# Optimization experiments

Measured on AMD Instinct MI355X. Metric: run time of the kernel, lower is better.

## Reference

```python
import jax, jax.numpy as jnp
import numpy as np
import math

B, S, D = 2, 2048, 2048
H, KVH, WIN = 16, 4, 256
HD = D // H            # 128
QPER = H // KVH        # 4


def setup_inputs() -> dict:
    key = jax.random.key(0)
    ks = jax.random.split(key, 9)
    s = lambda k, shp: jax.random.normal(k, shp, dtype=jnp.float32) * 0.02
    return {
        "x": jax.random.normal(ks[0], (B, S, D), dtype=jnp.float32),
        "Wq": s(ks[1], (D, D)),            "bq": jnp.zeros((D,), jnp.float32),
        "Wk": s(ks[2], (D, KVH * HD)),      "bk": jnp.zeros((KVH * HD,), jnp.float32),
        "Wv": s(ks[3], (D, KVH * HD)),      "bv": jnp.zeros((KVH * HD,), jnp.float32),
        "Wo": s(ks[4], (D, D)),            "bo": jnp.zeros((D,), jnp.float32),
    }


def reference(x, Wq, bq, Wk, bk, Wv, bv, Wo, bo):
    b, s, _ = x.shape
    # projections
    Q = (x @ Wq + bq).reshape(b, s, H, HD).transpose(0, 2, 1, 3)     # [b,H,s,hd]
    K = (x @ Wk + bk).reshape(b, s, KVH, HD).transpose(0, 2, 1, 3)   # [b,kvh,s,hd]
    V = (x @ Wv + bv).reshape(b, s, KVH, HD).transpose(0, 2, 1, 3)   # [b,kvh,s,hd]
    # GQA grouping: head h = g*QPER + q
    Qg = Q.reshape(b, KVH, QPER, s, HD)                               # [b,g,q,s,hd]
    scores = jnp.einsum('bgqsd,bgtd->bgqst', Qg, K)                   # [b,g,q,s,s]
    i = jnp.arange(s)[:, None]
    j = jnp.arange(s)[None, :]
    keep = (j <= i) & (j >= i - WIN + 1)                              # [s,s]
    scores = jnp.where(keep, scores, -jnp.inf)
    A = jax.nn.softmax(scores / math.sqrt(HD), axis=-1)
    O = jnp.einsum('bgqst,bgtd->bgqsd', A, V)                         # [b,g,q,s,hd]
    O = O.reshape(b, H, s, HD).transpose(0, 2, 1, 3).reshape(b, s, D)
    return O @ Wo + bo
```

## Files before the change

### kernel.cpp

```cpp
#include <hip/hip_runtime.h>
#include <hip/hip_bf16.h>
#include <math.h>

typedef __bf16 bf16_t;
typedef bf16_t bf16x8 __attribute__((ext_vector_type(8)));
typedef bf16_t bf16x4 __attribute__((ext_vector_type(4)));
typedef float  f32x4  __attribute__((ext_vector_type(4)));

#define NB    2
#define SEQ   2048
#define DIM   2048
#define NHEAD 16
#define NKVH  4
#define HDIM  128
#define WINSZ 256
#define KVD   512
#define QKVN  3072
#define MROWS 4096

__device__ __forceinline__ void async_copy16(const void* g, void* lds) {
    __builtin_amdgcn_global_load_lds(
        (const __attribute__((address_space(1))) void*)g,
        (__attribute__((address_space(3))) void*)lds,
        16, 0, 0);
}

__global__ __launch_bounds__(256) void preprocess(
    const float* __restrict__ x,  const float* __restrict__ Wq,
    const float* __restrict__ bq, const float* __restrict__ Wk,
    const float* __restrict__ bk, const float* __restrict__ Wv,
    const float* __restrict__ bv, const float* __restrict__ Wo,
    bf16_t* __restrict__ xb, bf16_t* __restrict__ WqkvT,
    bf16_t* __restrict__ WoT, float* __restrict__ bqkv) {
    __shared__ float tile[32][33];
    const int tid = threadIdx.x;
    int bid = blockIdx.x;
    if (bid < 8192) {
        int i = (bid * 256 + tid) * 4;
        float4 v = *(const float4*)(x + i);
        bf16x4 o;
        o[0] = (bf16_t)v.x; o[1] = (bf16_t)v.y; o[2] = (bf16_t)v.z; o[3] = (bf16_t)v.w;
        *(bf16x4*)(xb + i) = o;
        return;
    }
    bid -= 8192;
    const float* src; bf16_t* dst; int N;
    if (bid < 4096)       { src = Wq; dst = WqkvT;                          N = DIM; }
    else if (bid < 5120)  { src = Wk; dst = WqkvT + (size_t)DIM * DIM;      N = KVD; bid -= 4096; }
    else if (bid < 6144)  { src = Wv; dst = WqkvT + (size_t)(DIM+KVD)*DIM;  N = KVD; bid -= 5120; }
    else if (bid < 10240) { src = Wo; dst = WoT;                            N = DIM; bid -= 6144; }
    else {
        int i = (bid - 10240) * 256 + tid;
        if (i < QKVN) {
            float v = (i < DIM) ? bq[i] : ((i < DIM + KVD) ? bk[i - DIM] : bv[i - DIM - KVD]);
            bqkv[i] = v;
        }
        return;
    }
    const int K = DIM;
    int ntile = N / 32;
    int n0 = (bid % ntile) * 32, k0 = (bid / ntile) * 32;
    int tx = tid & 31, ty = tid >> 5;
    for (int r = ty; r < 32; r += 8)
        tile[r][tx] = src[(size_t)(k0 + r) * N + n0 + tx];
    __syncthreads();
    for (int r = ty; r < 32; r += 8)
        dst[(size_t)(n0 + r) * K + k0 + tx] = (bf16_t)tile[tx][r];
}

__global__ __launch_bounds__(256) void transpose_v(const bf16_t* __restrict__ QKV,
                                                   bf16_t* __restrict__ Vtb) {
    __shared__ bf16_t t[32][33];
    int tx = threadIdx.x & 31, ty = threadIdx.x >> 5;
    int jb = blockIdx.x, c0 = blockIdx.y * 32, b = blockIdx.z;
    int j0 = jb * 32;
    for (int r = ty; r < 32; r += 8)
        t[r][tx] = QKV[((size_t)(b * SEQ) + j0 + r) * QKVN + (DIM + KVD) + c0 + tx];
    __syncthreads();
    int g = c0 >> 7, dl = c0 & 127;
    bf16_t* outb = Vtb + (((size_t)(b * NKVH) + g) * 64 + jb) * 4096;
    for (int r = ty; r < 32; r += 8)
        outb[(dl + r) * 32 + tx] = t[tx][r];
}

template <int BM, int BN, typename OutT>
__global__ __launch_bounds__(512, 1) void gemm8p(const bf16_t* __restrict__ A,
                                                 const bf16_t* __restrict__ Bt,
                                                 const float* __restrict__ bias,
                                                 OutT* __restrict__ C,
                                                 int M, int N, int K, float qs, int qcols) {
    constexpr int ASLOTS = BM / 16;
    constexpr int BSLOTS = BN / 16;
    constexpr int MF   = BM / 32;
    constexpr int NF   = BN / 64;
    constexpr int AHALF = BM * 32;
    constexpr int BHALF = BN * 32;
    constexpr int BUFSZ = 2 * (AHALF + BHALF);
    __shared__ bf16_t lds[2 * BUFSZ];

    const int tid  = threadIdx.x;
    const int wave = tid >> 6;
    const int lane = tid & 63;
    const int lg = lane >> 4, lc = lane & 15;
    const int wr = wave >> 2, wc = wave & 3;

    const int nbn  = N / BN;
    const int nblk = (M / BM) * nbn;
    const int qq   = nblk >> 3;
    const int swz  = (blockIdx.x & 7) * qq + (blockIdx.x >> 3);
    const long brow = (long)(swz / nbn) * BM;
    const long bcol = (long)(swz % nbn) * BN;

    const int aiss = (ASLOTS - wave + 7) >> 3;
    const int biss = (BSLOTS - wave + 7) >> 3;
    const int miss = aiss + biss;

    f32x4 acc[MF][NF] = {};

    auto stage = [&](int buf, int p, int kt) {
        const int kcol = kt * 64 + p * 32;
        const int srow = lane >> 2;
        const int sch  = lane & 3;
        {
            bf16_t* d = lds + buf * BUFSZ + p * AHALF;
#pragma unroll
            for (int s = wave; s < ASLOTS; s += 8) {
                int row = s * 16 + srow;
                int ch  = sch ^ ((row >> 1) & 3);
                async_copy16(A + (brow + row) * (long)K + kcol + ch * 8, d + s * 512);
            }
        }
        {
            bf16_t* d = lds + buf * BUFSZ + 2 * AHALF + p * BHALF;
#pragma unroll
            for (int s = wave; s < BSLOTS; s += 8) {
                int row = s * 16 + srow;
                int ch  = sch ^ ((row >> 1) & 3);
                async_copy16(Bt + (bcol + row) * (long)K + kcol + ch * 8, d + s * 512);
            }
        }
    };

    stage(0, 0, 0);
    stage(0, 1, 0);

    const int NT = K >> 6;
    const int cswz = (lg ^ ((lc >> 1) & 3)) * 8;
    for (int t = 0; t < NT; ++t) {
#pragma unroll
        for (int p = 0; p < 2; ++p) {
            if (t == NT - 1 && p == 1) {
                asm volatile("s_waitcnt vmcnt(0)" ::: "memory");
            } else if (miss == 4) {
                asm volatile("s_waitcnt vmcnt(4)" ::: "memory");
            } else if (miss == 3) {
                asm volatile("s_waitcnt vmcnt(3)" ::: "memory");
            } else {
                asm volatile("s_waitcnt vmcnt(2)" ::: "memory");
            }
            __builtin_amdgcn_s_barrier();
            asm volatile("" ::: "memory");
            const bf16_t* Ab = lds + (t & 1) * BUFSZ + p * AHALF;
            const bf16_t* Bb = lds + (t & 1) * BUFSZ + 2 * AHALF + p * BHALF;
            bf16x8 af[MF], bv[NF];
#pragma unroll
            for (int m = 0; m < MF; ++m)
                af[m] = *(const bf16x8*)(Ab + (wr * (BM / 2) + m * 16 + lc) * 32 + cswz);
#pragma unroll
            for (int n = 0; n < NF; ++n)
                bv[n] = *(const bf16x8*)(Bb + (wc * (BN / 4) + n * 16 + lc) * 32 + cswz);
            if (t + 1 < NT) stage((t + 1) & 1, p, t + 1);
            __builtin_amdgcn_s_setprio(1);
#pragma unroll
            for (int m = 0; m < MF; ++m)
#pragma unroll
                for (int n = 0; n < NF; ++n)
                    acc[m][n] = __builtin_amdgcn_mfma_f32_16x16x32_bf16(af[m], bv[n], acc[m][n], 0, 0, 0);
            __builtin_amdgcn_s_setprio(0);
        }
    }

#pragma unroll
    for (int n = 0; n < NF; ++n) {
        int gc = (int)bcol + wc * (BN / 4) + n * 16 + lc;
        float bvs = bias[gc];
        bool ds = gc < qcols;
#pragma unroll
        for (int m = 0; m < MF; ++m) {
            long gr = brow + wr * (BM / 2) + m * 16 + 4 * lg;
#pragma unroll
            for (int r = 0; r < 4; ++r) {
                float v = acc[m][n][r] + bvs;
                if (ds) v *= qs;
                C[(gr + r) * (long)N + gc] = (OutT)v;
            }
        }
    }
}

__global__ __launch_bounds__(256) void attn_kernel(const bf16_t* __restrict__ QKV,
                                                   const bf16_t* __restrict__ Vtb,
                                                   bf16_t* __restrict__ Ob) {
    __shared__ bf16_t Kls[2][32 * 128];
    __shared__ bf16_t Vls[2][128 * 32];
    __shared__ bf16_t Pls[4][32 * 40];

    const int wv   = threadIdx.x >> 6;
    const int lane = threadIdx.x & 63;
    const int lg = lane >> 4, lc = lane & 15;

    const int swb = (blockIdx.x & 7) * 64 + (blockIdx.x >> 3);
    const int ti = swb & 63;
    const int g  = (swb >> 6) & 3;
    const int b  = swb >> 8;
    const int h  = g * 4 + wv;
    const int i0 = ti * 32;
    bf16_t* P = &Pls[wv][0];

    bf16x8 qf[2][4];
#pragma unroll
    for (int sq = 0; sq < 2; ++sq) {
        const bf16_t* qp = QKV + ((size_t)(b * SEQ) + i0 + sq * 16 + lc) * QKVN + h * HDIM + lg * 8;
#pragma unroll
        for (int kk = 0; kk < 4; ++kk) qf[sq][kk] = *(const bf16x8*)(qp + kk * 32);
    }

    auto stage = [&](int buf, int jb) {
        const int j0s = jb * 32;
        const bf16_t* kgb = QKV + ((size_t)(b * SEQ) + j0s) * QKVN + DIM + g * HDIM;
#pragma unroll
        for (int ii = 0; ii < 2; ++ii) {
            int i = wv * 2 + ii;
            int row = i * 4 + (lane >> 4);
            int ch  = (lane & 15) ^ (row & 7);
            async_copy16(kgb + (size_t)row * QKVN + ch * 8, &Kls[buf][i * 512]);
        }
        const bf16_t* vgb = Vtb + (((size_t)(b * NKVH) + g) * 64 + jb) * 4096;
#pragma unroll
        for (int ii = 0; ii < 2; ++ii) {
            int i = wv * 2 + ii;
            int row = i * 16 + (lane >> 2);
            int ch  = (lane & 3) ^ ((row ^ (row >> 2)) & 3);
            async_copy16(vgb + row * 32 + ch * 8, &Vls[buf][i * 512]);
        }
    };

    float m_run[2] = {-1e30f, -1e30f}, l_run[2] = {0.f, 0.f};
    f32x4 oacc[2][8] = {};

    int jlo = i0 - (WINSZ - 1); if (jlo < 0) jlo = 0;
    const int jb0 = jlo >> 5;
    const int jb1 = (i0 + 31) >> 5;

    stage(0, jb0);

    for (int jb = jb0; jb <= jb1; ++jb) {
        const int j0 = jb * 32;
        const int cur = (jb - jb0) & 1;
        asm volatile("s_waitcnt vmcnt(0)" ::: "memory");
        __builtin_amdgcn_s_barrier();
        asm volatile("" ::: "memory");

        bf16x8 kf[2][4];
#pragma unroll
        for (int t = 0; t < 2; ++t)
#pragma unroll
            for (int kk = 0; kk < 4; ++kk) {
                int row = t * 16 + lc;
                int ch  = (kk * 4 + lg) ^ (row & 7);
                kf[t][kk] = *(const bf16x8*)(&Kls[cur][row * 128 + ch * 8]);
            }
        if (jb < jb1) stage(cur ^ 1, jb + 1);
        asm volatile("s_waitcnt lgkmcnt(0)" ::: "memory");
        __builtin_amdgcn_sched_barrier(0);

        f32x4 s[2][2];
        __builtin_amdgcn_s_setprio(1);
#pragma unroll
        for (int t = 0; t < 2; ++t)
#pragma unroll
            for (int sq = 0; sq < 2; ++sq) {
                f32x4 sv = {};
#pragma unroll
                for (int kk = 0; kk < 4; ++kk)
                    sv = __builtin_amdgcn_mfma_f32_16x16x32_bf16(kf[t][kk], qf[sq][kk], sv, 0, 0, 0);
                s[t][sq] = sv;
            }
        __builtin_amdgcn_s_setprio(0);

        const bool edge = (j0 < i0 - (WINSZ - 32)) || (j0 > i0 - 31);
        if (edge) {
#pragma unroll
            for (int t = 0; t < 2; ++t)
#pragma unroll
                for (int sq = 0; sq < 2; ++sq) {
                    int irow = i0 + sq * 16 + lc;
#pragma unroll
                    for (int r = 0; r < 4; ++r) {
                        int j = j0 + t * 16 + 4 * lg + r;
                        if (j > irow || j < irow - (WINSZ - 1)) s[t][sq][r] = -1e30f;
                    }
                }
        }
        float tmax[2];
#pragma unroll
        for (int sq = 0; sq < 2; ++sq) {
            float tm = fmaxf(fmaxf(fmaxf(s[0][sq][0], s[0][sq][1]), fmaxf(s[0][sq][2], s[0][sq][3])),
                             fmaxf(fmaxf(s[1][sq][0], s[1][sq][1]), fmaxf(s[1][sq][2], s[1][sq][3])));
            tm = fmaxf(tm, __shfl_xor(tm, 16, 64));
            tm = fmaxf(tm, __shfl_xor(tm, 32, 64));
            tmax[sq] = tm;
        }
        if (!__all(tmax[0] - m_run[0] <= 8.0f && tmax[1] - m_run[1] <= 8.0f)) {
#pragma unroll
            for (int sq = 0; sq < 2; ++sq) {
                float m_new = fmaxf(m_run[sq], tmax[sq]);
                float resc = __builtin_amdgcn_exp2f(m_run[sq] - m_new);
                l_run[sq] *= resc;
#pragma unroll
                for (int c = 0; c < 8; ++c) {
                    oacc[sq][c][0] *= resc; oacc[sq][c][1] *= resc;
                    oacc[sq][c][2] *= resc; oacc[sq][c][3] *= resc;
                }
                m_run[sq] = m_new;
            }
        }
        float psum[2] = {0.f, 0.f};
#pragma unroll
        for (int t = 0; t < 2; ++t)
#pragma unroll
            for (int sq = 0; sq < 2; ++sq) {
                bf16x4 pk;
#pragma unroll
                for (int r = 0; r < 4; ++r) {
                    float sv = s[t][sq][r];
                    float p = (edge && sv < -5e29f) ? 0.f : __builtin_amdgcn_exp2f(sv - m_run[sq]);
                    psum[sq] += p;
                    pk[r] = (bf16_t)p;
                }
                *(bf16x4*)(P + (sq * 16 + lc) * 40 + t * 16 + lg * 4) = pk;
            }
#pragma unroll
        for (int sq = 0; sq < 2; ++sq) {
            float ps = psum[sq];
            ps += __shfl_xor(ps, 16, 64);
            ps += __shfl_xor(ps, 32, 64);
            l_run[sq] += ps;
        }
        asm volatile("" ::: "memory");

        bf16x8 vf[8];
#pragma unroll
        for (int c = 0; c < 8; ++c) {
            int row = c * 16 + lc;
            int ch  = lg ^ ((row ^ (row >> 2)) & 3);
            vf[c] = *(const bf16x8*)(&Vls[cur][row * 32 + ch * 8]);
        }
        bf16x8 pf[2];
#pragma unroll
        for (int sq = 0; sq < 2; ++sq)
            pf[sq] = *(const bf16x8*)(P + (sq * 16 + lc) * 40 + lg * 8);

        __builtin_amdgcn_s_setprio(1);
#pragma unroll
        for (int c = 0; c < 8; ++c)
#pragma unroll
            for (int sq = 0; sq < 2; ++sq)
                oacc[sq][c] = __builtin_amdgcn_mfma_f32_16x16x32_bf16(vf[c], pf[sq], oacc[sq][c], 0, 0, 0);
        __builtin_amdgcn_s_setprio(0);
    }

#pragma unroll
    for (int sq = 0; sq < 2; ++sq) {
        const float inv = 1.f / l_run[sq];
#pragma unroll
        for (int c = 0; c < 8; ++c) {
            bf16x4 ov;
#pragma unroll
            for (int r = 0; r < 4; ++r) ov[r] = (bf16_t)(oacc[sq][c][r] * inv);
            *(bf16x4*)(Ob + ((size_t)(b * SEQ) + i0 + sq * 16 + lc) * DIM + h * HDIM + c * 16 + lg * 4) = ov;
        }
    }
}

extern "C" void kernel_launch(void* const* d_in, const int* in_sizes, int n_in,
                              void* d_out, int out_size, void* d_ws, size_t ws_size,
                              hipStream_t stream) {
    const float* x  = (const float*)d_in[0];
    const float* Wq = (const float*)d_in[1];
    const float* bq = (const float*)d_in[2];
    const float* Wk = (const float*)d_in[3];
    const float* bk = (const float*)d_in[4];
    const float* Wv = (const float*)d_in[5];
    const float* bv = (const float*)d_in[6];
    const float* Wo = (const float*)d_in[7];
    const float* bo = (const float*)d_in[8];
    float* out = (float*)d_out;

    char* ws = (char*)d_ws;
    bf16_t* xb    = (bf16_t*)(ws);
    bf16_t* WqkvT = (bf16_t*)(ws + (16u << 20));
    bf16_t* WoT   = (bf16_t*)(ws + (28u << 20));
    bf16_t* QKVb  = (bf16_t*)(ws + (36u << 20));
    float*  bqkv  = (float*) (ws + (60u << 20));
    bf16_t* Vtb   = WqkvT;
    bf16_t* Ob    = xb;

    const float qs = 0.12751707498038074f;

    preprocess<<<18444, 256, 0, stream>>>(x, Wq, bq, Wk, bk, Wv, bv, Wo,
                                          xb, WqkvT, WoT, bqkv);

    gemm8p<256, 192, bf16_t><<<dim3((MROWS / 256) * (QKVN / 192)), 512, 0, stream>>>(
        xb, WqkvT, bqkv, QKVb, MROWS, QKVN, DIM, qs, DIM);

    transpose_v<<<dim3(SEQ / 32, KVD / 32, NB), 256, 0, stream>>>(QKVb, Vtb);

    attn_kernel<<<dim3(NB * NKVH * (SEQ / 32)), 256, 0, stream>>>(QKVb, Vtb, Ob);

    gemm8p<128, 256, float><<<dim3((MROWS / 128) * (DIM / 256)), 512, 0, stream>>>(
        Ob, WoT, bo, out, MROWS, DIM, DIM, 1.0f, 0);
}
```

Baseline: 147.6 us.

## Replace large-tile GEMM with 128x128 triple-buffered multi-block GEMM

Both projection GEMMs move from one 512-thread block per CU with 256x192 or 128x256 tiles and double buffering to 256-thread blocks with 128x128 tiles, K-step 32, a three-stage LDS ring, and three blocks per CU. The goal is more blocks in flight and deeper prefetch to hide load latency, and better wave balance across CUs. The cost is lower per-block data reuse, so more global and L2 traffic per FLOP and more barriers per unit of work.

```diff
diff --git a/kernel.cpp b/kernel.cpp
--- a/kernel.cpp
+++ b/kernel.cpp
@@ -83,111 +83,79 @@
         outb[(dl + r) * 32 + tx] = t[tx][r];
 }
 
-template <int BM, int BN, typename OutT>
-__global__ __launch_bounds__(512, 1) void gemm8p(const bf16_t* __restrict__ A,
+template <typename OutT>
+__global__ __launch_bounds__(256, 3) void gemm3b(const bf16_t* __restrict__ A,
                                                  const bf16_t* __restrict__ Bt,
                                                  const float* __restrict__ bias,
                                                  OutT* __restrict__ C,
                                                  int M, int N, int K, float qs, int qcols) {
-    constexpr int ASLOTS = BM / 16;
-    constexpr int BSLOTS = BN / 16;
-    constexpr int MF   = BM / 32;
-    constexpr int NF   = BN / 64;
-    constexpr int AHALF = BM * 32;
-    constexpr int BHALF = BN * 32;
-    constexpr int BUFSZ = 2 * (AHALF + BHALF);
-    __shared__ bf16_t lds[2 * BUFSZ];
-
-    const int tid  = threadIdx.x;
-    const int wave = tid >> 6;
-    const int lane = tid & 63;
+    __shared__ bf16_t lds[3][8192];
+    const int tid = threadIdx.x, wave = tid >> 6, lane = tid & 63;
     const int lg = lane >> 4, lc = lane & 15;
-    const int wr = wave >> 2, wc = wave & 3;
-
-    const int nbn  = N / BN;
-    const int nblk = (M / BM) * nbn;
-    const int qq   = nblk >> 3;
-    const int swz  = (blockIdx.x & 7) * qq + (blockIdx.x >> 3);
-    const long brow = (long)(swz / nbn) * BM;
-    const long bcol = (long)(swz % nbn) * BN;
-
-    const int aiss = (ASLOTS - wave + 7) >> 3;
-    const int biss = (BSLOTS - wave + 7) >> 3;
-    const int miss = aiss + biss;
-
-    f32x4 acc[MF][NF] = {};
-
-    auto stage = [&](int buf, int p, int kt) {
-        const int kcol = kt * 64 + p * 32;
-        const int srow = lane >> 2;
-        const int sch  = lane & 3;
-        {
-            bf16_t* d = lds + buf * BUFSZ + p * AHALF;
-#pragma unroll
-            for (int s = wave; s < ASLOTS; s += 8) {
-                int row = s * 16 + srow;
-                int ch  = sch ^ ((row >> 1) & 3);
-                async_copy16(A + (brow + row) * (long)K + kcol + ch * 8, d + s * 512);
-            }
-        }
-        {
-            bf16_t* d = lds + buf * BUFSZ + 2 * AHALF + p * BHALF;
-#pragma unroll
-            for (int s = wave; s < BSLOTS; s += 8) {
-                int row = s * 16 + srow;
-                int ch  = sch ^ ((row >> 1) & 3);
-                async_copy16(Bt + (bcol + row) * (long)K + kcol + ch * 8, d + s * 512);
-            }
+    const int wr = wave >> 1, wc = wave & 1;
+    const int nbn = N >> 7, nblk = (M >> 7) * nbn, qq = nblk >> 3;
+    const int swz = (blockIdx.x & 7) * qq + (blockIdx.x >> 3);
+    const long brow = (long)(swz / nbn) << 7;
+    const long bcol = (long)(swz % nbn) << 7;
+    const int srow = tid >> 2;
+    const int sch  = tid & 3;
+    const int cswz = (lg ^ ((lc >> 1) & 3)) * 8;
+
+    f32x4 acc[4][4] = {};
+
+    auto stage = [&](int buf, int kt) {
+        const long kc = (long)kt * 32;
+#pragma unroll
+        for (int h = 0; h < 2; ++h) {
+            int row = h * 64 + srow;
+            int ch  = sch ^ ((row >> 1) & 3);
+            async_copy16(A + (brow + row) * (long)K + kc + ch * 8,
+                         &lds[buf][h * 2048 + tid * 8]);
+        }
+#pragma unroll
+        for (int h = 0; h < 2; ++h) {
+            int row = h * 64 + srow;
+            int ch  = sch ^ ((row >> 1) & 3);
+            async_copy16(Bt + (bcol + row) * (long)K + kc + ch * 8,
+                         &lds[buf][4096 + h * 2048 + tid * 8]);
         }
     };
 
-    stage(0, 0, 0);
-    stage(0, 1, 0);
-
-    const int NT = K >> 6;
-    const int cswz = (lg ^ ((lc >> 1) & 3)) * 8;
+    const int NT = K >> 5;
+    stage(0, 0);
+    stage(1, 1);
+
     for (int t = 0; t < NT; ++t) {
-#pragma unroll
-        for (int p = 0; p < 2; ++p) {
-            if (t == NT - 1 && p == 1) {
-                asm volatile("s_waitcnt vmcnt(0)" ::: "memory");
-            } else if (miss == 4) {
-                asm volatile("s_waitcnt vmcnt(4)" ::: "memory");
-            } else if (miss == 3) {
-                asm volatile("s_waitcnt vmcnt(3)" ::: "memory");
-            } else {
-                asm volatile("s_waitcnt vmcnt(2)" ::: "memory");
-            }
-            __builtin_amdgcn_s_barrier();
-            asm volatile("" ::: "memory");
-            const bf16_t* Ab = lds + (t & 1) * BUFSZ + p * AHALF;
-            const bf16_t* Bb = lds + (t & 1) * BUFSZ + 2 * AHALF + p * BHALF;
-            bf16x8 af[MF], bv[NF];
-#pragma unroll
-            for (int m = 0; m < MF; ++m)
-                af[m] = *(const bf16x8*)(Ab + (wr * (BM / 2) + m * 16 + lc) * 32 + cswz);
-#pragma unroll
-            for (int n = 0; n < NF; ++n)
-                bv[n] = *(const bf16x8*)(Bb + (wc * (BN / 4) + n * 16 + lc) * 32 + cswz);
-            if (t + 1 < NT) stage((t + 1) & 1, p, t + 1);
-            __builtin_amdgcn_s_setprio(1);
-#pragma unroll
-            for (int m = 0; m < MF; ++m)
-#pragma unroll
-                for (int n = 0; n < NF; ++n)
-                    acc[m][n] = __builtin_amdgcn_mfma_f32_16x16x32_bf16(af[m], bv[n], acc[m][n], 0, 0, 0);
-            __builtin_amdgcn_s_setprio(0);
-        }
-    }
-
-#pragma unroll
-    for (int n = 0; n < NF; ++n) {
-        int gc = (int)bcol + wc * (BN / 4) + n * 16 + lc;
+        if (t == NT - 1) asm volatile("s_waitcnt vmcnt(0)" ::: "memory");
+        else             asm volatile("s_waitcnt vmcnt(4)" ::: "memory");
+        __builtin_amdgcn_s_barrier();
+        asm volatile("" ::: "memory");
+        if (t + 2 < NT) stage((t + 2) % 3, t + 2);
+        const bf16_t* buf = &lds[t % 3][0];
+        bf16x8 af[4], bv[4];
+#pragma unroll
+        for (int m = 0; m < 4; ++m)
+            af[m] = *(const bf16x8*)(buf + (wr * 64 + m * 16 + lc) * 32 + cswz);
+#pragma unroll
+        for (int n = 0; n < 4; ++n)
+            bv[n] = *(const bf16x8*)(buf + 4096 + (wc * 64 + n * 16 + lc) * 32 + cswz);
+        __builtin_amdgcn_s_setprio(1);
+#pragma unroll
+        for (int m = 0; m < 4; ++m)
+#pragma unroll
+            for (int n = 0; n < 4; ++n)
+                acc[m][n] = __builtin_amdgcn_mfma_f32_16x16x32_bf16(af[m], bv[n], acc[m][n], 0, 0, 0);
+        __builtin_amdgcn_s_setprio(0);
+    }
+
+#pragma unroll
+    for (int n = 0; n < 4; ++n) {
+        int gc = (int)bcol + wc * 64 + n * 16 + lc;
         float bvs = bias[gc];
         bool ds = gc < qcols;
 #pragma unroll
-        for (int m = 0; m < MF; ++m) {
-            long gr = brow + wr * (BM / 2) + m * 16 + 4 * lg;
+        for (int m = 0; m < 4; ++m) {
+            long gr = brow + wr * 64 + m * 16 + 4 * lg;
 #pragma unroll
             for (int r = 0; r < 4; ++r) {
                 float v = acc[m][n][r] + bvs;
@@ -411,13 +379,13 @@
     preprocess<<<18444, 256, 0, stream>>>(x, Wq, bq, Wk, bk, Wv, bv, Wo,
                                           xb, WqkvT, WoT, bqkv);
 
-    gemm8p<256, 192, bf16_t><<<dim3((MROWS / 256) * (QKVN / 192)), 512, 0, stream>>>(
+    gemm3b<bf16_t><<<dim3((MROWS / 128) * (QKVN / 128)), 256, 0, stream>>>(
         xb, WqkvT, bqkv, QKVb, MROWS, QKVN, DIM, qs, DIM);
 
     transpose_v<<<dim3(SEQ / 32, KVD / 32, NB), 256, 0, stream>>>(QKVb, Vtb);
 
     attn_kernel<<<dim3(NB * NKVH * (SEQ / 32)), 256, 0, stream>>>(QKVb, Vtb, Ob);
 
-    gemm8p<128, 256, float><<<dim3((MROWS / 128) * (DIM / 256)), 512, 0, stream>>>(
+    gemm3b<float><<<dim3((MROWS / 128) * (DIM / 128)), 256, 0, stream>>>(
         Ob, WoT, bo, out, MROWS, DIM, DIM, 1.0f, 0);
 }
```

After: 160.5 us. 1.09x slower.

## Fuse V transpose into QKV GEMM epilogue and triple-buffer attention K/V loads

Applied to the files above, without the earlier changes.

The QKV GEMM epilogue now writes the V columns straight into the blocked, transposed Vtb layout, so the separate transpose_v kernel and its extra read and write of V are gone. The attention kernel moves from double to triple buffering of K/V tiles, prefetching two blocks ahead and waiting with a partial vmcnt so loads overlap more with compute. This costs more LDS per block, which may lower occupancy, and the epilogue stores to Vtb are scattered 8-byte writes. Vtb also moves to its own workspace region.

```diff
diff --git a/kernel.cpp b/kernel.cpp
--- a/kernel.cpp
+++ b/kernel.cpp
@@ -68,26 +68,12 @@
         dst[(size_t)(n0 + r) * K + k0 + tx] = (bf16_t)tile[tx][r];
 }
 
-__global__ __launch_bounds__(256) void transpose_v(const bf16_t* __restrict__ QKV,
-                                                   bf16_t* __restrict__ Vtb) {
-    __shared__ bf16_t t[32][33];
-    int tx = threadIdx.x & 31, ty = threadIdx.x >> 5;
-    int jb = blockIdx.x, c0 = blockIdx.y * 32, b = blockIdx.z;
-    int j0 = jb * 32;
-    for (int r = ty; r < 32; r += 8)
-        t[r][tx] = QKV[((size_t)(b * SEQ) + j0 + r) * QKVN + (DIM + KVD) + c0 + tx];
-    __syncthreads();
-    int g = c0 >> 7, dl = c0 & 127;
-    bf16_t* outb = Vtb + (((size_t)(b * NKVH) + g) * 64 + jb) * 4096;
-    for (int r = ty; r < 32; r += 8)
-        outb[(dl + r) * 32 + tx] = t[tx][r];
-}
-
-template <int BM, int BN, typename OutT>
+template <int BM, int BN, typename OutT, bool VFUSE>
 __global__ __launch_bounds__(512, 1) void gemm8p(const bf16_t* __restrict__ A,
                                                  const bf16_t* __restrict__ Bt,
                                                  const float* __restrict__ bias,
                                                  OutT* __restrict__ C,
+                                                 bf16_t* __restrict__ vtb,
                                                  int M, int N, int K, float qs, int qcols) {
     constexpr int ASLOTS = BM / 16;
     constexpr int BSLOTS = BN / 16;
@@ -184,6 +170,24 @@
     for (int n = 0; n < NF; ++n) {
         int gc = (int)bcol + wc * (BN / 4) + n * 16 + lc;
         float bvs = bias[gc];
+        if constexpr (VFUSE) {
+            if (gc >= DIM + KVD) {
+                int vg = (gc - (DIM + KVD)) >> 7;
+                int dl = (gc - (DIM + KVD)) & 127;
+#pragma unroll
+                for (int m = 0; m < MF; ++m) {
+                    long gr = brow + wr * (BM / 2) + m * 16 + 4 * lg;
+                    int bb = (int)(gr >> 11);
+                    int js = (int)(gr & (SEQ - 1));
+                    bf16x4 ov;
+#pragma unroll
+                    for (int r = 0; r < 4; ++r) ov[r] = (bf16_t)(acc[m][n][r] + bvs);
+                    *(bf16x4*)(vtb + (((size_t)(bb * NKVH) + vg) * 64 + (js >> 5)) * 4096
+                                   + dl * 32 + (js & 31)) = ov;
+                }
+                continue;
+            }
+        }
         bool ds = gc < qcols;
 #pragma unroll
         for (int m = 0; m < MF; ++m) {
@@ -201,8 +205,8 @@
 __global__ __launch_bounds__(256) void attn_kernel(const bf16_t* __restrict__ QKV,
                                                    const bf16_t* __restrict__ Vtb,
                                                    bf16_t* __restrict__ Ob) {
-    __shared__ bf16_t Kls[2][32 * 128];
-    __shared__ bf16_t Vls[2][128 * 32];
+    __shared__ bf16_t Kls[3][32 * 128];
+    __shared__ bf16_t Vls[3][128 * 32];
     __shared__ bf16_t Pls[4][32 * 40];
 
     const int wv   = threadIdx.x >> 6;
@@ -253,11 +257,14 @@
     const int jb1 = (i0 + 31) >> 5;
 
     stage(0, jb0);
+    if (jb0 + 1 <= jb1) stage(1, jb0 + 1);
 
     for (int jb = jb0; jb <= jb1; ++jb) {
         const int j0 = jb * 32;
-        const int cur = (jb - jb0) & 1;
-        asm volatile("s_waitcnt vmcnt(0)" ::: "memory");
+        const int it = jb - jb0;
+        const int cur = it % 3;
+        if (jb < jb1) asm volatile("s_waitcnt vmcnt(4)" ::: "memory");
+        else          asm volatile("s_waitcnt vmcnt(0)" ::: "memory");
         __builtin_amdgcn_s_barrier();
         asm volatile("" ::: "memory");
 
@@ -270,7 +277,7 @@
                 int ch  = (kk * 4 + lg) ^ (row & 7);
                 kf[t][kk] = *(const bf16x8*)(&Kls[cur][row * 128 + ch * 8]);
             }
-        if (jb < jb1) stage(cur ^ 1, jb + 1);
+        if (jb + 2 <= jb1) stage((it + 2) % 3, jb + 2);
         asm volatile("s_waitcnt lgkmcnt(0)" ::: "memory");
         __builtin_amdgcn_sched_barrier(0);
 
@@ -403,7 +410,7 @@
     bf16_t* WoT   = (bf16_t*)(ws + (28u << 20));
     bf16_t* QKVb  = (bf16_t*)(ws + (36u << 20));
     float*  bqkv  = (float*) (ws + (60u << 20));
-    bf16_t* Vtb   = WqkvT;
+    bf16_t* Vtb   = (bf16_t*)(ws + (61u << 20));
     bf16_t* Ob    = xb;
 
     const float qs = 0.12751707498038074f;
@@ -411,13 +418,11 @@
     preprocess<<<18444, 256, 0, stream>>>(x, Wq, bq, Wk, bk, Wv, bv, Wo,
                                           xb, WqkvT, WoT, bqkv);
 
-    gemm8p<256, 192, bf16_t><<<dim3((MROWS / 256) * (QKVN / 192)), 512, 0, stream>>>(
-        xb, WqkvT, bqkv, QKVb, MROWS, QKVN, DIM, qs, DIM);
-
-    transpose_v<<<dim3(SEQ / 32, KVD / 32, NB), 256, 0, stream>>>(QKVb, Vtb);
+    gemm8p<256, 192, bf16_t, true><<<dim3((MROWS / 256) * (QKVN / 192)), 512, 0, stream>>>(
+        xb, WqkvT, bqkv, QKVb, Vtb, MROWS, QKVN, DIM, qs, DIM);
 
     attn_kernel<<<dim3(NB * NKVH * (SEQ / 32)), 256, 0, stream>>>(QKVb, Vtb, Ob);
 
-    gemm8p<128, 256, float><<<dim3((MROWS / 128) * (DIM / 256)), 512, 0, stream>>>(
-        Ob, WoT, bo, out, MROWS, DIM, DIM, 1.0f, 0);
+    gemm8p<128, 256, float, false><<<dim3((MROWS / 128) * (DIM / 256)), 512, 0, stream>>>(
+        Ob, WoT, bo, out, nullptr, MROWS, DIM, DIM, 1.0f, 0);
 }
```

After: 143.2 us. 3.0% less time.
